# Kernel tuning notes

Hardware: AMD Instinct MI355X
Metric: run time of the kernel (lower is better)

Reference implementation:

```python
import jax, jax.numpy as jnp
import numpy as np
import math

B, L, E, H = 4, 1024, 1024, 16
D = E // H  # head_dim = 64
SCALE = 8.0
EPS = 1e-6

def setup_inputs() -> dict:
    key = jax.random.key(0)
    ks = jax.random.split(key, 16)
    def xavier(k, shape):
        fan_in, fan_out = shape[1], shape[0]
        a = math.sqrt(6.0 / (fan_in + fan_out))
        return jax.random.uniform(k, shape, jnp.float32, -a, a)
    return {
        "query": jax.random.normal(ks[0], (B, L, E), jnp.float32),
        "key": jax.random.normal(ks[1], (B, L, E), jnp.float32),
        "value": jax.random.normal(ks[2], (B, L, E), jnp.float32),
        "attn_mask": jax.random.uniform(ks[3], (B, L), jnp.float32),
        "key_padding_mask": jax.random.randint(ks[4], (B, L), 0, 2) > 0,
        "Wq": xavier(ks[5], (E, E)), "bq": jnp.zeros((E,), jnp.float32),
        "Wk": xavier(ks[6], (E, E)), "bk": jnp.zeros((E,), jnp.float32),
        "Wv": xavier(ks[7], (E, E)), "bv": jnp.zeros((E,), jnp.float32),
        "Wo": xavier(ks[8], (E, E)), "bo": jnp.zeros((E,), jnp.float32),
    }

def reference(query, key, value, attn_mask, key_padding_mask,
              Wq, bq, Wk, bk, Wv, bv, Wo, bo):
    # projections (torch Linear: x @ W.T + b)
    q = (query @ Wq.T + bq).reshape(B, L, H, D).transpose(0, 2, 1, 3)  # (B,H,L,D)
    k = (key @ Wk.T + bk).reshape(B, L, H, D).transpose(0, 2, 1, 3)
    v = (value @ Wv.T + bv).reshape(B, L, H, D).transpose(0, 2, 1, 3)
    scores = jnp.einsum('bhqd,bhkd->bhqk', q, k) / math.sqrt(D)  # (B,H,L,L)
    # soft log-mask bias (training path: no hard -inf at mask==0)
    log_mask = jnp.log(jnp.clip(attn_mask, EPS))  # (B,L)
    scores = scores + SCALE * log_mask[:, None, None, :]
    # key padding mask -> -inf
    scores = jnp.where(key_padding_mask[:, None, None, :], -jnp.inf, scores)
    attn_weights = jax.nn.softmax(scores, axis=-1)  # dropout p=0 -> identity
    attn_output = jnp.einsum('bhqk,bhkd->bhqd', attn_weights, v)
    attn_output = attn_output.transpose(0, 2, 1, 3).reshape(B, L, E)
    attn_output = attn_output @ Wo.T + bo
    return attn_output, attn_weights.mean(axis=1)
```

## Files before the change

### kernel.cpp

```cpp
#include <hip/hip_runtime.h>
#include <math.h>

#define Bsz 4
#define Lq  1024
#define Emb 1024
#define Hh  16
#define Dd  64

typedef short bf16x8 __attribute__((ext_vector_type(8)));
typedef float f32x4 __attribute__((ext_vector_type(4)));

static __device__ __forceinline__ unsigned short f2bf(float f) {
    unsigned u = __float_as_uint(f);
    return (unsigned short)((u + 0x7FFFu + ((u >> 16) & 1u)) >> 16);
}
static __device__ __forceinline__ unsigned pack2(float lo, float hi) {
    return __builtin_amdgcn_perm(__float_as_uint(hi) + 0x8000u,
                                 __float_as_uint(lo) + 0x8000u, 0x07060302u);
}

static __device__ __forceinline__ float cross_max(float x) {
    x = fmaxf(x, __shfl_xor(x, 16, 64));
    x = fmaxf(x, __shfl_xor(x, 32, 64));
    return x;
}
static __device__ __forceinline__ float cross_sum(float x) {
    x += __shfl_xor(x, 16, 64);
    x += __shfl_xor(x, 32, 64);
    return x;
}

#define GLOAD_LDS16(gp, lp) __builtin_amdgcn_global_load_lds(                  \
    (const __attribute__((address_space(1))) void*)(gp),                       \
    (__attribute__((address_space(3))) void*)(lp), 16, 0, 0)

__global__ __launch_bounds__(256) void bias_kernel(const float* __restrict__ mask,
                                                   const int* __restrict__ kpm,
                                                   float* __restrict__ bias, int n)
{
    int i = blockIdx.x * 256 + threadIdx.x;
    if (i < n) {
        float b = 8.0f * logf(fmaxf(mask[i], 1e-6f));
        bias[i] = kpm[i] ? -INFINITY : b;
    }
}

__global__ __launch_bounds__(256) void cvt_qkv(const float* __restrict__ q,
                                               const float* __restrict__ k,
                                               const float* __restrict__ v,
                                               unsigned short* __restrict__ qo,
                                               unsigned short* __restrict__ ko,
                                               unsigned short* __restrict__ vo)
{
    int i = blockIdx.x * 256 + threadIdx.x;
    const float* src; unsigned short* dst; int off;
    if (i < 1048576)      { src = q; dst = qo; off = i; }
    else if (i < 2097152) { src = k; dst = ko; off = i - 1048576; }
    else                  { src = v; dst = vo; off = i - 2097152; }
    float4 x = ((const float4*)src)[off];
    ushort4 o;
    o.x = f2bf(x.x); o.y = f2bf(x.y); o.z = f2bf(x.z); o.w = f2bf(x.w);
    ((ushort4*)dst)[off] = o;
}

__global__ __launch_bounds__(256) void cvt_w4(const float* __restrict__ w0,
                                              const float* __restrict__ w1,
                                              const float* __restrict__ w2,
                                              const float* __restrict__ w3,
                                              unsigned short* __restrict__ o0,
                                              unsigned short* __restrict__ o1,
                                              unsigned short* __restrict__ o2,
                                              unsigned short* __restrict__ o3)
{
    int i = blockIdx.x * 256 + threadIdx.x;
    int reg = i >> 18, off = i & 262143;
    const float* src = (reg == 0) ? w0 : (reg == 1) ? w1 : (reg == 2) ? w2 : w3;
    unsigned short* dst = (reg == 0) ? o0 : (reg == 1) ? o1 : (reg == 2) ? o2 : o3;
    float4 x = ((const float4*)src)[off];
    ushort4 o;
    o.x = f2bf(x.x); o.y = f2bf(x.y); o.z = f2bf(x.z); o.w = f2bf(x.w);
    ((ushort4*)dst)[off] = o;
}

__global__ __launch_bounds__(256) void gemm_qkv(const unsigned short* __restrict__ Aq,
                                                const unsigned short* __restrict__ Ak,
                                                const unsigned short* __restrict__ Av,
                                                const unsigned short* __restrict__ Wq,
                                                const unsigned short* __restrict__ Wk,
                                                const unsigned short* __restrict__ Wv,
                                                const float* __restrict__ biq,
                                                const float* __restrict__ bik,
                                                const float* __restrict__ biv,
                                                unsigned short* __restrict__ Oq,
                                                unsigned short* __restrict__ Ok,
                                                unsigned short* __restrict__ Ov)
{
    const int K = 1024;
    __shared__ unsigned short sA[64][32];
    __shared__ unsigned short sB[128][32];
    int tid = threadIdx.x;
    int w = tid >> 6, lane = tid & 63;

    int bid = blockIdx.x;
    int which = bid >> 9;
    int lin = bid & 511;
    int xcd = lin & 7, idx = lin >> 3;
    int bm = (xcd * 8 + (idx >> 3)) * 64;
    int bn = (idx & 7) * 128;

    const unsigned short* A = (which == 0) ? Aq : (which == 1) ? Ak : Av;
    const unsigned short* Bw = (which == 0) ? Wq : (which == 1) ? Wk : Wv;
    const float* bias = (which == 0) ? biq : (which == 1) ? bik : biv;
    unsigned short* outp = (which == 0) ? Oq : (which == 1) ? Ok : Ov;

    int wr = (w >> 1) * 32, wc = (w & 1) * 64;
    int fr = lane & 15, fk = (lane >> 4) * 8;

    const unsigned short* Ag = A + (size_t)(bm + w * 16 + (lane >> 2)) * K + (lane & 3) * 8;
    const unsigned short* Bg = Bw + (size_t)(bn + w * 32 + (lane >> 2)) * K + (lane & 3) * 8;
    unsigned short* lA0 = &sA[w * 16][0];
    unsigned short* lB0 = &sB[w * 32][0];
    unsigned short* lB1 = &sB[w * 32 + 16][0];

    f32x4 acc[2][4];
#pragma unroll
    for (int i = 0; i < 2; ++i)
#pragma unroll
        for (int j = 0; j < 4; ++j) acc[i][j] = (f32x4){0.f, 0.f, 0.f, 0.f};

    for (int k0 = 0; k0 < K; k0 += 32) {
        __syncthreads();
        GLOAD_LDS16(Ag + k0,          lA0);
        GLOAD_LDS16(Bg + k0,          lB0);
        GLOAD_LDS16(Bg + 16 * K + k0, lB1);
        __syncthreads();
        bf16x8 af[2], bfv[4];
#pragma unroll
        for (int i = 0; i < 2; ++i) af[i]  = *(const bf16x8*)&sA[wr + i * 16 + fr][fk];
#pragma unroll
        for (int j = 0; j < 4; ++j) bfv[j] = *(const bf16x8*)&sB[wc + j * 16 + fr][fk];
#pragma unroll
        for (int i = 0; i < 2; ++i)
#pragma unroll
            for (int j = 0; j < 4; ++j)
                acc[i][j] = __builtin_amdgcn_mfma_f32_16x16x32_bf16(af[i], bfv[j], acc[i][j], 0, 0, 0);
    }

    int rb = (lane >> 4) * 4;
#pragma unroll
    for (int j = 0; j < 4; ++j) {
        int n = bn + wc + j * 16 + fr;
        float bia = bias[n];
#pragma unroll
        for (int i = 0; i < 2; ++i) {
#pragma unroll
            for (int r = 0; r < 4; ++r) {
                int m = bm + wr + i * 16 + rb + r;
                float v = acc[i][j][r] + bia;
                int b = m >> 10, l = m & 1023, h = n >> 6, d = n & 63;
                if (which == 2)
                    outp[(((size_t)(b * Hh + h)) * Dd + d) * Lq + l] = f2bf(v);
                else
                    outp[(((size_t)(b * Hh + h)) * Lq + l) * Dd + d] = f2bf(v);
            }
        }
    }
}

__global__ __launch_bounds__(256) void gemm_o(const unsigned short* __restrict__ A,
                                              const unsigned short* __restrict__ Bw,
                                              const float* __restrict__ bias,
                                              float* __restrict__ outp)
{
    const int K = 1024;
    __shared__ unsigned short sA[64][32];
    __shared__ unsigned short sB[128][32];
    int tid = threadIdx.x;
    int w = tid >> 6, lane = tid & 63;

    int lin = blockIdx.x;
    int xcd = lin & 7, idx = lin >> 3;
    int bm = (xcd * 8 + (idx >> 3)) * 64;
    int bn = (idx & 7) * 128;

    int wr = (w >> 1) * 32, wc = (w & 1) * 64;
    int fr = lane & 15, fk = (lane >> 4) * 8;

    const unsigned short* Ag = A + (size_t)(bm + w * 16 + (lane >> 2)) * K + (lane & 3) * 8;
    const unsigned short* Bg = Bw + (size_t)(bn + w * 32 + (lane >> 2)) * K + (lane & 3) * 8;
    unsigned short* lA0 = &sA[w * 16][0];
    unsigned short* lB0 = &sB[w * 32][0];
    unsigned short* lB1 = &sB[w * 32 + 16][0];

    f32x4 acc[2][4];
#pragma unroll
    for (int i = 0; i < 2; ++i)
#pragma unroll
        for (int j = 0; j < 4; ++j) acc[i][j] = (f32x4){0.f, 0.f, 0.f, 0.f};

    for (int k0 = 0; k0 < K; k0 += 32) {
        __syncthreads();
        GLOAD_LDS16(Ag + k0,          lA0);
        GLOAD_LDS16(Bg + k0,          lB0);
        GLOAD_LDS16(Bg + 16 * K + k0, lB1);
        __syncthreads();
        bf16x8 af[2], bfv[4];
#pragma unroll
        for (int i = 0; i < 2; ++i) af[i]  = *(const bf16x8*)&sA[wr + i * 16 + fr][fk];
#pragma unroll
        for (int j = 0; j < 4; ++j) bfv[j] = *(const bf16x8*)&sB[wc + j * 16 + fr][fk];
#pragma unroll
        for (int i = 0; i < 2; ++i)
#pragma unroll
            for (int j = 0; j < 4; ++j)
                acc[i][j] = __builtin_amdgcn_mfma_f32_16x16x32_bf16(af[i], bfv[j], acc[i][j], 0, 0, 0);
    }

    int rb = (lane >> 4) * 4;
#pragma unroll
    for (int j = 0; j < 4; ++j) {
        int n = bn + wc + j * 16 + fr;
        float bia = bias[n];
#pragma unroll
        for (int i = 0; i < 2; ++i)
#pragma unroll
            for (int r = 0; r < 4; ++r) {
                int m = bm + wr + i * 16 + rb + r;
                outp[(size_t)m * 1024 + n] = acc[i][j][r] + bia;
            }
    }
}

__global__ __launch_bounds__(256) void attn_flash(const unsigned short* __restrict__ Qh,
                                                  const unsigned short* __restrict__ Kh,
                                                  const unsigned short* __restrict__ Vt,
                                                  const float* __restrict__ mbias,
                                                  unsigned short* __restrict__ ctx,
                                                  float* __restrict__ mstats,
                                                  float* __restrict__ lstats)
{
    __shared__ float sBias[1024];
    __shared__ unsigned short Wl[4][2][16][64];
    __shared__ unsigned short Kl[2][64][64];
    __shared__ unsigned short Vl[2][64][64];

    int tid = threadIdx.x;
    int w = tid >> 6, lane = tid & 63;
    int fr = lane & 15, fg = lane >> 4;

    int lin = blockIdx.x;
    int xcd = lin & 7, jj = lin >> 3;
    int pair = xcd * 8 + (jj >> 3);
    int qt = jj & 7;
    int b = pair & 3, h = pair >> 2;

    int q0A = qt * 128 + w * 32;
    int q0B = q0A + 16;
    int swz = (fr & 7) << 2;
    int csw = fr & 7;

    const unsigned short* Qp = Qh + ((size_t)(b * Hh + h)) * Lq * Dd;
    const unsigned short* Kp = Kh + ((size_t)(b * Hh + h)) * Lq * Dd;
    const unsigned short* Vp = Vt + ((size_t)(b * Hh + h)) * Dd * Lq;

    int srl = lane >> 3;
    int scb = (lane & 7) ^ srl;

#define STAGEK(BUF, KC) do {                                                     \
    _Pragma("unroll")                                                            \
    for (int i = 0; i < 2; ++i)                                                  \
        GLOAD_LDS16(Kp + (size_t)((KC) + w * 16 + i * 8 + srl) * Dd + scb * 8,   \
                    &Kl[BUF][w * 16 + i * 8][0]);                                \
} while (0)
#define STAGEV(BUF, KC) do {                                                     \
    _Pragma("unroll")                                                            \
    for (int i = 0; i < 2; ++i)                                                  \
        GLOAD_LDS16(Vp + (size_t)(w * 16 + i * 8 + srl) * Lq + (KC) + scb * 8,   \
                    &Vl[BUF][w * 16 + i * 8][0]);                                \
} while (0)

    for (int i = tid; i < 1024; i += 256) sBias[i] = mbias[b * Lq + i];

    bf16x8 qA0 = *(const bf16x8*)(Qp + (size_t)(q0A + fr) * Dd + fg * 8);
    bf16x8 qA1 = *(const bf16x8*)(Qp + (size_t)(q0A + fr) * Dd + 32 + fg * 8);
    bf16x8 qB0 = *(const bf16x8*)(Qp + (size_t)(q0B + fr) * Dd + fg * 8);
    bf16x8 qB1 = *(const bf16x8*)(Qp + (size_t)(q0B + fr) * Dd + 32 + fg * 8);

    f32x4 OA[4], OB[4];
#pragma unroll
    for (int dt = 0; dt < 4; ++dt) { OA[dt] = (f32x4){0.f,0.f,0.f,0.f}; OB[dt] = (f32x4){0.f,0.f,0.f,0.f}; }
    float mA = -INFINITY, lA = 0.f, mB = -INFINITY, lB = 0.f;

    bf16x8 vb0[4], vb1[4];

#define RDK(K0, K1, BUF) do {                                                    \
    _Pragma("unroll")                                                            \
    for (int kt = 0; kt < 4; ++kt) {                                             \
        K0[kt] = *(const bf16x8*)&Kl[BUF][kt * 16 + fr][(fg ^ csw) * 8];         \
        K1[kt] = *(const bf16x8*)&Kl[BUF][kt * 16 + fr][((4 + fg) ^ csw) * 8];   \
    }                                                                            \
} while (0)
#define RDV(BUF) do {                                                            \
    _Pragma("unroll")                                                            \
    for (int dt = 0; dt < 4; ++dt) {                                             \
        vb0[dt] = *(const bf16x8*)&Vl[BUF][dt * 16 + fr][(fg ^ csw) * 8];        \
        vb1[dt] = *(const bf16x8*)&Vl[BUF][dt * 16 + fr][((4 + fg) ^ csw) * 8];  \
    }                                                                            \
} while (0)

#define QK(S, K0, K1, B0, B1) do {                                               \
    _Pragma("unroll")                                                            \
    for (int kt = 0; kt < 4; ++kt) {                                             \
        S[kt] = __builtin_amdgcn_mfma_f32_16x16x32_bf16(K0[kt], B0, (f32x4){0.f,0.f,0.f,0.f}, 0, 0, 0); \
        S[kt] = __builtin_amdgcn_mfma_f32_16x16x32_bf16(K1[kt], B1, S[kt], 0, 0, 0); \
    }                                                                            \
} while (0)

#define SMPV(S, MT, LT, OT, TI, KC) do {                                         \
    float v_[16];                                                                \
    _Pragma("unroll")                                                            \
    for (int kt = 0; kt < 4; ++kt) {                                             \
        float4 bb = *(const float4*)&sBias[(KC) + kt * 16 + fg * 4];             \
        _Pragma("unroll")                                                        \
        for (int r = 0; r < 4; ++r)                                              \
            v_[kt * 4 + r] = S[kt][r] * 0.125f + (&bb.x)[r];                     \
    }                                                                            \
    float t8[8];                                                                 \
    _Pragma("unroll")                                                            \
    for (int i = 0; i < 8; ++i) t8[i] = fmaxf(v_[i], v_[i + 8]);                 \
    float t4[4];                                                                 \
    _Pragma("unroll")                                                            \
    for (int i = 0; i < 4; ++i) t4[i] = fmaxf(t8[i], t8[i + 4]);                 \
    float pmax = fmaxf(fmaxf(t4[0], t4[1]), fmaxf(t4[2], t4[3]));                \
    pmax = cross_max(pmax);                                                      \
    float mn = fmaxf(MT, pmax);                                                  \
    float sc = __expf(MT - mn);                                                  \
    _Pragma("unroll")                                                            \
    for (int i = 0; i < 16; ++i) v_[i] = __expf(v_[i] - mn);                     \
    _Pragma("unroll")                                                            \
    for (int i = 0; i < 8; ++i) t8[i] = v_[i] + v_[i + 8];                       \
    _Pragma("unroll")                                                            \
    for (int i = 0; i < 4; ++i) t4[i] = t8[i] + t8[i + 4];                       \
    float cs = (t4[0] + t4[1]) + (t4[2] + t4[3]);                                \
    cs = cross_sum(cs);                                                          \
    LT = LT * sc + cs;                                                           \
    MT = mn;                                                                     \
    _Pragma("unroll")                                                            \
    for (int dt = 0; dt < 4; ++dt)                                               \
        _Pragma("unroll")                                                        \
        for (int r = 0; r < 4; ++r) OT[dt][r] *= sc;                             \
    _Pragma("unroll")                                                            \
    for (int kt = 0; kt < 4; ++kt) {                                             \
        unsigned w0 = pack2(v_[kt * 4 + 0], v_[kt * 4 + 1]);                     \
        unsigned w1 = pack2(v_[kt * 4 + 2], v_[kt * 4 + 3]);                     \
        uint2 pr; pr.x = w0; pr.y = w1;                                          \
        *(uint2*)&Wl[w][TI][fr][2 * ((kt * 8 + fg * 2) ^ swz)] = pr;             \
    }                                                                            \
    bf16x8 pa0 = *(const bf16x8*)&Wl[w][TI][fr][2 * ((fg * 4) ^ swz)];           \
    bf16x8 pa1 = *(const bf16x8*)&Wl[w][TI][fr][2 * ((16 + fg * 4) ^ swz)];      \
    _Pragma("unroll")                                                            \
    for (int dt = 0; dt < 4; ++dt) {                                             \
        OT[dt] = __builtin_amdgcn_mfma_f32_16x16x32_bf16(vb0[dt], pa0, OT[dt], 0, 0, 0); \
        OT[dt] = __builtin_amdgcn_mfma_f32_16x16x32_bf16(vb1[dt], pa1, OT[dt], 0, 0, 0); \
    }                                                                            \
} while (0)

    STAGEK(0, 0);
    STAGEV(0, 0);
    __syncthreads();

#pragma unroll 1
    for (int c = 0; c < 16; ++c) {
        int cur = c & 1;
        if (c < 15) {
            STAGEK(cur ^ 1, (c + 1) * 64);
            STAGEV(cur ^ 1, (c + 1) * 64);
        }
        bf16x8 k0[4], k1[4];
        RDK(k0, k1, cur);
        f32x4 SA[4], SB[4];
        QK(SA, k0, k1, qA0, qA1);
        QK(SB, k0, k1, qB0, qB1);
        RDV(cur);
        SMPV(SA, mA, lA, OA, 0, c * 64);
        SMPV(SB, mB, lB, OB, 1, c * 64);
        __syncthreads();
    }
#undef STAGEK
#undef STAGEV
#undef RDK
#undef RDV
#undef QK
#undef SMPV

    float liA = 1.f / lA, liB = 1.f / lB;
#pragma unroll
    for (int dt = 0; dt < 4; ++dt) {
#pragma unroll
        for (int r = 0; r < 4; ++r) { OA[dt][r] *= liA; OB[dt][r] *= liB; }
    }
#pragma unroll
    for (int dt = 0; dt < 4; ++dt) {
        uint2 pa; pa.x = pack2(OA[dt][0], OA[dt][1]); pa.y = pack2(OA[dt][2], OA[dt][3]);
        *(uint2*)(ctx + ((size_t)(b * Lq + q0A + fr)) * Emb + h * Dd + dt * 16 + fg * 4) = pa;
        uint2 pb; pb.x = pack2(OB[dt][0], OB[dt][1]); pb.y = pack2(OB[dt][2], OB[dt][3]);
        *(uint2*)(ctx + ((size_t)(b * Lq + q0B + fr)) * Emb + h * Dd + dt * 16 + fg * 4) = pb;
    }

    if (lane < 16) {
        mstats[(size_t)(b * Hh + h) * Lq + q0A + lane] = mA;
        lstats[(size_t)(b * Hh + h) * Lq + q0A + lane] = liA;
        mstats[(size_t)(b * Hh + h) * Lq + q0B + lane] = mB;
        lstats[(size_t)(b * Hh + h) * Lq + q0B + lane] = liB;
    }
}

__global__ __launch_bounds__(256) void attn_out2(const unsigned short* __restrict__ Qh,
                                                 const unsigned short* __restrict__ Kh,
                                                 const float* __restrict__ mbias,
                                                 const float* __restrict__ mstats,
                                                 const float* __restrict__ lstats,
                                                 float* __restrict__ out2)
{
    __shared__ unsigned short sQ[2][32][64];
    __shared__ unsigned short sK[2][128][64];
    __shared__ float sM[16][32];
    __shared__ float sLi[16][32];

    int tid = threadIdx.x;
    int w = tid >> 6, lane = tid & 63;
    int fr = lane & 15, fg = lane >> 4;
    int q0 = blockIdx.x * 32;
    int kc = blockIdx.y * 128;
    int b  = blockIdx.z;

    for (int i = tid; i < 512; i += 256) {
        int h = i >> 5, qq = i & 31;
        sM[h][qq]  = mstats[(size_t)(b * Hh + h) * Lq + q0 + qq];
        sLi[h][qq] = lstats[(size_t)(b * Hh + h) * Lq + q0 + qq];
    }

    int srl = lane >> 3;
    int scb = (lane & 7) ^ srl;
    int csw = fr & 7;

#define STAGEH(BUF, H) do {                                                      \
    const unsigned short* Qp_ = Qh + ((size_t)(b * Hh + (H))) * Lq * Dd;         \
    const unsigned short* Kp_ = Kh + ((size_t)(b * Hh + (H))) * Lq * Dd;         \
    GLOAD_LDS16(Qp_ + (size_t)(q0 + w * 8 + srl) * Dd + scb * 8, &sQ[BUF][w * 8][0]); \
    _Pragma("unroll")                                                            \
    for (int i = 0; i < 4; ++i)                                                  \
        GLOAD_LDS16(Kp_ + (size_t)(kc + w * 32 + i * 8 + srl) * Dd + scb * 8,    \
                    &sK[BUF][w * 32 + i * 8][0]);                                \
} while (0)

#define RDH(AQ, BKk, BUF) do {                                                   \
    _Pragma("unroll")                                                            \
    for (int rt = 0; rt < 2; ++rt)                                               \
        _Pragma("unroll")                                                        \
        for (int ks = 0; ks < 2; ++ks)                                           \
            AQ[rt][ks] = *(const bf16x8*)&sQ[BUF][rt * 16 + fr][((ks * 4 + fg) ^ csw) * 8]; \
    _Pragma("unroll")                                                            \
    for (int ct = 0; ct < 2; ++ct)                                               \
        _Pragma("unroll")                                                        \
        for (int ks = 0; ks < 2; ++ks)                                           \
            BKk[ct][ks] = *(const bf16x8*)&sK[BUF][w * 32 + ct * 16 + fr][((ks * 4 + fg) ^ csw) * 8]; \
} while (0)

#define COMPH(AQ, BKk, H) do {                                                   \
    float4 mrow[2], lirow[2];                                                    \
    _Pragma("unroll")                                                            \
    for (int rt = 0; rt < 2; ++rt) {                                             \
        mrow[rt]  = *(const float4*)&sM[(H)][rt * 16 + fg * 4];                  \
        lirow[rt] = *(const float4*)&sLi[(H)][rt * 16 + fg * 4];                 \
    }                                                                            \
    _Pragma("unroll")                                                            \
    for (int rt = 0; rt < 2; ++rt)                                               \
        _Pragma("unroll")                                                        \
        for (int ct = 0; ct < 2; ++ct) {                                         \
            f32x4 s_ = __builtin_amdgcn_mfma_f32_16x16x32_bf16(AQ[rt][0], BKk[ct][0], (f32x4){0.f,0.f,0.f,0.f}, 0, 0, 0); \
            s_ = __builtin_amdgcn_mfma_f32_16x16x32_bf16(AQ[rt][1], BKk[ct][1], s_, 0, 0, 0); \
            float bia = ct ? bias1 : bias0;                                      \
            _Pragma("unroll")                                                    \
            for (int r = 0; r < 4; ++r)                                          \
                o2[rt][ct][r] += __expf(s_[r] * 0.125f + bia - mrow[rt][r]) * lirow[rt][r]; \
        }                                                                        \
} while (0)

    float bias0 = mbias[b * Lq + kc + w * 32 + fr];
    float bias1 = mbias[b * Lq + kc + w * 32 + 16 + fr];

    float o2[2][2][4];
#pragma unroll
    for (int rt = 0; rt < 2; ++rt)
#pragma unroll
        for (int ct = 0; ct < 2; ++ct)
#pragma unroll
            for (int r = 0; r < 4; ++r) o2[rt][ct][r] = 0.f;

    STAGEH(0, 0);
    __syncthreads();

#pragma unroll 1
    for (int h = 0; h < Hh; ++h) {
        int cur = h & 1;
        if (h < Hh - 1) STAGEH(cur ^ 1, h + 1);
        bf16x8 aq[2][2], bk[2][2];
        RDH(aq, bk, cur);
        COMPH(aq, bk, h);
        __syncthreads();
    }
#undef STAGEH
#undef RDH
#undef COMPH

#pragma unroll
    for (int rt = 0; rt < 2; ++rt)
#pragma unroll
        for (int ct = 0; ct < 2; ++ct)
#pragma unroll
            for (int r = 0; r < 4; ++r)
                out2[((size_t)(b * Lq + q0 + rt * 16 + fg * 4 + r)) * Lq + kc + w * 32 + ct * 16 + fr]
                    = o2[rt][ct][r] * 0.0625f;
}

extern "C" void kernel_launch(void* const* d_in, const int* in_sizes, int n_in,
                              void* d_out, int out_size, void* d_ws, size_t ws_size,
                              hipStream_t stream)
{
    const float* query = (const float*)d_in[0];
    const float* key   = (const float*)d_in[1];
    const float* value = (const float*)d_in[2];
    const float* amask = (const float*)d_in[3];
    const int*   kpm   = (const int*)d_in[4];
    const float* Wq = (const float*)d_in[5];
    const float* bq = (const float*)d_in[6];
    const float* Wk = (const float*)d_in[7];
    const float* bk = (const float*)d_in[8];
    const float* Wv = (const float*)d_in[9];
    const float* bv = (const float*)d_in[10];
    const float* Wo = (const float*)d_in[11];
    const float* bo = (const float*)d_in[12];

    float* out1 = (float*)d_out;
    float* out2 = out1 + (size_t)Bsz * Lq * Emb;

    const size_t MB = 1u << 20;
    char* ws = (char*)d_ws;
    unsigned short* qbf = (unsigned short*)(ws + 0 * MB);
    unsigned short* kbf = (unsigned short*)(ws + 8 * MB);
    unsigned short* vbf = (unsigned short*)(ws + 16 * MB);
    unsigned short* wqb = (unsigned short*)(ws + 24 * MB);
    unsigned short* wkb = (unsigned short*)(ws + 26 * MB);
    unsigned short* wvb = (unsigned short*)(ws + 28 * MB);
    unsigned short* wob = (unsigned short*)(ws + 30 * MB);
    unsigned short* QhB = (unsigned short*)(ws + 32 * MB);
    unsigned short* KhB = (unsigned short*)(ws + 40 * MB);
    unsigned short* VtB = (unsigned short*)(ws + 48 * MB);
    unsigned short* ctxB = (unsigned short*)(ws + 56 * MB);
    float* mbias  = (float*)(ws + 64 * MB);
    float* mstats = (float*)(ws + 0 * MB);
    float* lstats = (float*)(ws + 0 * MB + 256 * 1024);

    bias_kernel<<<16, 256, 0, stream>>>(amask, kpm, mbias, Bsz * Lq);

    cvt_qkv<<<12288, 256, 0, stream>>>(query, key, value, qbf, kbf, vbf);
    cvt_w4<<<4096, 256, 0, stream>>>(Wq, Wk, Wv, Wo, wqb, wkb, wvb, wob);

    gemm_qkv<<<1536, 256, 0, stream>>>(qbf, kbf, vbf, wqb, wkb, wvb,
                                       bq, bk, bv, QhB, KhB, VtB);

    attn_flash<<<512, 256, 0, stream>>>(QhB, KhB, VtB, mbias, ctxB, mstats, lstats);
    attn_out2<<<dim3(32, 8, 4), 256, 0, stream>>>(QhB, KhB, mbias, mstats, lstats, out2);

    gemm_o<<<512, 256, 0, stream>>>(ctxB, wob, bo, out1);
}
```

Before: 171.3 us.

## Double-buffer projection GEMMs with BK=64 and XOR-swizzled LDS layout

```diff
diff --git a/kernel.cpp b/kernel.cpp
--- a/kernel.cpp
+++ b/kernel.cpp
@@ -96,8 +96,8 @@
                                                 unsigned short* __restrict__ Ov)
 {
     const int K = 1024;
-    __shared__ unsigned short sA[64][32];
-    __shared__ unsigned short sB[128][32];
+    __shared__ unsigned short sA[2][64][64];
+    __shared__ unsigned short sB[2][128][64];
     int tid = threadIdx.x;
     int w = tid >> 6, lane = tid & 63;
 
@@ -114,13 +114,23 @@
     unsigned short* outp = (which == 0) ? Oq : (which == 1) ? Ok : Ov;
 
     int wr = (w >> 1) * 32, wc = (w & 1) * 64;
-    int fr = lane & 15, fk = (lane >> 4) * 8;
-
-    const unsigned short* Ag = A + (size_t)(bm + w * 16 + (lane >> 2)) * K + (lane & 3) * 8;
-    const unsigned short* Bg = Bw + (size_t)(bn + w * 32 + (lane >> 2)) * K + (lane & 3) * 8;
-    unsigned short* lA0 = &sA[w * 16][0];
-    unsigned short* lB0 = &sB[w * 32][0];
-    unsigned short* lB1 = &sB[w * 32 + 16][0];
+    int fr = lane & 15, fg = lane >> 4;
+    int csw = fr & 7;
+
+    int srl = lane >> 3;
+    int scb = (lane & 7) ^ srl;
+
+    const unsigned short* Ag = A + (size_t)(bm + w * 16 + srl) * K + scb * 8;
+    const unsigned short* Bg = Bw + (size_t)(bn + w * 32 + srl) * K + scb * 8;
+
+#define STAGE(BUF, K0) do {                                                      \
+    _Pragma("unroll")                                                            \
+    for (int j = 0; j < 2; ++j)                                                  \
+        GLOAD_LDS16(Ag + (size_t)j * 8 * K + (K0), &sA[BUF][w * 16 + j * 8][0]); \
+    _Pragma("unroll")                                                            \
+    for (int j = 0; j < 4; ++j)                                                  \
+        GLOAD_LDS16(Bg + (size_t)j * 8 * K + (K0), &sB[BUF][w * 32 + j * 8][0]); \
+} while (0)
 
     f32x4 acc[2][4];
 #pragma unroll
@@ -128,23 +138,34 @@
 #pragma unroll
         for (int j = 0; j < 4; ++j) acc[i][j] = (f32x4){0.f, 0.f, 0.f, 0.f};
 
-    for (int k0 = 0; k0 < K; k0 += 32) {
+    STAGE(0, 0);
+    __syncthreads();
+
+#pragma unroll 1
+    for (int k0 = 0; k0 < K; k0 += 64) {
+        int cur = (k0 >> 6) & 1;
+        if (k0 + 64 < K) STAGE(cur ^ 1, k0 + 64);
+        bf16x8 af[2][2], bfv[4][2];
+#pragma unroll
+        for (int i = 0; i < 2; ++i)
+#pragma unroll
+            for (int kk = 0; kk < 2; ++kk)
+                af[i][kk] = *(const bf16x8*)&sA[cur][wr + i * 16 + fr][((kk * 4 + fg) ^ csw) * 8];
+#pragma unroll
+        for (int j = 0; j < 4; ++j)
+#pragma unroll
+            for (int kk = 0; kk < 2; ++kk)
+                bfv[j][kk] = *(const bf16x8*)&sB[cur][wc + j * 16 + fr][((kk * 4 + fg) ^ csw) * 8];
+#pragma unroll
+        for (int i = 0; i < 2; ++i)
+#pragma unroll
+            for (int j = 0; j < 4; ++j) {
+                acc[i][j] = __builtin_amdgcn_mfma_f32_16x16x32_bf16(af[i][0], bfv[j][0], acc[i][j], 0, 0, 0);
+                acc[i][j] = __builtin_amdgcn_mfma_f32_16x16x32_bf16(af[i][1], bfv[j][1], acc[i][j], 0, 0, 0);
+            }
         __syncthreads();
-        GLOAD_LDS16(Ag + k0,          lA0);
-        GLOAD_LDS16(Bg + k0,          lB0);
-        GLOAD_LDS16(Bg + 16 * K + k0, lB1);
-        __syncthreads();
-        bf16x8 af[2], bfv[4];
-#pragma unroll
-        for (int i = 0; i < 2; ++i) af[i]  = *(const bf16x8*)&sA[wr + i * 16 + fr][fk];
-#pragma unroll
-        for (int j = 0; j < 4; ++j) bfv[j] = *(const bf16x8*)&sB[wc + j * 16 + fr][fk];
-#pragma unroll
-        for (int i = 0; i < 2; ++i)
-#pragma unroll
-            for (int j = 0; j < 4; ++j)
-                acc[i][j] = __builtin_amdgcn_mfma_f32_16x16x32_bf16(af[i], bfv[j], acc[i][j], 0, 0, 0);
-    }
+    }
+#undef STAGE
 
     int rb = (lane >> 4) * 4;
 #pragma unroll
@@ -173,8 +194,8 @@
                                               float* __restrict__ outp)
 {
     const int K = 1024;
-    __shared__ unsigned short sA[64][32];
-    __shared__ unsigned short sB[128][32];
+    __shared__ unsigned short sA[2][64][64];
+    __shared__ unsigned short sB[2][128][64];
     int tid = threadIdx.x;
     int w = tid >> 6, lane = tid & 63;
 
@@ -184,13 +205,23 @@
     int bn = (idx & 7) * 128;
 
     int wr = (w >> 1) * 32, wc = (w & 1) * 64;
-    int fr = lane & 15, fk = (lane >> 4) * 8;
-
-    const unsigned short* Ag = A + (size_t)(bm + w * 16 + (lane >> 2)) * K + (lane & 3) * 8;
-    const unsigned short* Bg = Bw + (size_t)(bn + w * 32 + (lane >> 2)) * K + (lane & 3) * 8;
-    unsigned short* lA0 = &sA[w * 16][0];
-    unsigned short* lB0 = &sB[w * 32][0];
-    unsigned short* lB1 = &sB[w * 32 + 16][0];
+    int fr = lane & 15, fg = lane >> 4;
+    int csw = fr & 7;
+
+    int srl = lane >> 3;
+    int scb = (lane & 7) ^ srl;
+
+    const unsigned short* Ag = A + (size_t)(bm + w * 16 + srl) * K + scb * 8;
+    const unsigned short* Bg = Bw + (size_t)(bn + w * 32 + srl) * K + scb * 8;
+
+#define STAGE(BUF, K0) do {                                                      \
+    _Pragma("unroll")                                                            \
+    for (int j = 0; j < 2; ++j)                                                  \
+        GLOAD_LDS16(Ag + (size_t)j * 8 * K + (K0), &sA[BUF][w * 16 + j * 8][0]); \
+    _Pragma("unroll")                                                            \
+    for (int j = 0; j < 4; ++j)                                                  \
+        GLOAD_LDS16(Bg + (size_t)j * 8 * K + (K0), &sB[BUF][w * 32 + j * 8][0]); \
+} while (0)
 
     f32x4 acc[2][4];
 #pragma unroll
@@ -198,23 +229,34 @@
 #pragma unroll
         for (int j = 0; j < 4; ++j) acc[i][j] = (f32x4){0.f, 0.f, 0.f, 0.f};
 
-    for (int k0 = 0; k0 < K; k0 += 32) {
+    STAGE(0, 0);
+    __syncthreads();
+
+#pragma unroll 1
+    for (int k0 = 0; k0 < K; k0 += 64) {
+        int cur = (k0 >> 6) & 1;
+        if (k0 + 64 < K) STAGE(cur ^ 1, k0 + 64);
+        bf16x8 af[2][2], bfv[4][2];
+#pragma unroll
+        for (int i = 0; i < 2; ++i)
+#pragma unroll
+            for (int kk = 0; kk < 2; ++kk)
+                af[i][kk] = *(const bf16x8*)&sA[cur][wr + i * 16 + fr][((kk * 4 + fg) ^ csw) * 8];
+#pragma unroll
+        for (int j = 0; j < 4; ++j)
+#pragma unroll
+            for (int kk = 0; kk < 2; ++kk)
+                bfv[j][kk] = *(const bf16x8*)&sB[cur][wc + j * 16 + fr][((kk * 4 + fg) ^ csw) * 8];
+#pragma unroll
+        for (int i = 0; i < 2; ++i)
+#pragma unroll
+            for (int j = 0; j < 4; ++j) {
+                acc[i][j] = __builtin_amdgcn_mfma_f32_16x16x32_bf16(af[i][0], bfv[j][0], acc[i][j], 0, 0, 0);
+                acc[i][j] = __builtin_amdgcn_mfma_f32_16x16x32_bf16(af[i][1], bfv[j][1], acc[i][j], 0, 0, 0);
+            }
         __syncthreads();
-        GLOAD_LDS16(Ag + k0,          lA0);
-        GLOAD_LDS16(Bg + k0,          lB0);
-        GLOAD_LDS16(Bg + 16 * K + k0, lB1);
-        __syncthreads();
-        bf16x8 af[2], bfv[4];
-#pragma unroll
-        for (int i = 0; i < 2; ++i) af[i]  = *(const bf16x8*)&sA[wr + i * 16 + fr][fk];
-#pragma unroll
-        for (int j = 0; j < 4; ++j) bfv[j] = *(const bf16x8*)&sB[wc + j * 16 + fr][fk];
-#pragma unroll
-        for (int i = 0; i < 2; ++i)
-#pragma unroll
-            for (int j = 0; j < 4; ++j)
-                acc[i][j] = __builtin_amdgcn_mfma_f32_16x16x32_bf16(af[i], bfv[j], acc[i][j], 0, 0, 0);
-    }
+    }
+#undef STAGE
 
     int rb = (lane >> 4) * 4;
 #pragma unroll
```

Result: faster. 160.4 us (-6.4%).
